# Kernel tuning notes

Measured on AMD Instinct MI355X. Metric: run time of the kernel, lower is better.

Reference implementation:

```python
import jax, jax.numpy as jnp
import numpy as np

N = 128
INSTANCES = 64
EMBED_DIM = 256
HIDDEN = 1024
BATCH = 2048


def _kaiming(key, dims):
    # matches custom_kaiming: randn * sqrt(2 / dims[-2])
    return jax.random.normal(key, dims, dtype=jnp.float32) * np.sqrt(2.0 / float(dims[-2])).astype(np.float32)


def setup_inputs() -> dict:
    key = jax.random.key(0)
    k_a, k_el, k_er, k_lin, k_un = jax.random.split(key, 5)
    a = jax.random.randint(k_a, (BATCH, 2), 0, N, dtype=jnp.int64 if jax.config.jax_enable_x64 else jnp.int32)
    return {
        "a": a,
        "embedding_left": _kaiming(k_el, (INSTANCES, N, EMBED_DIM)),
        "embedding_right": _kaiming(k_er, (INSTANCES, N, EMBED_DIM)),
        "linear": _kaiming(k_lin, (INSTANCES, EMBED_DIM, HIDDEN)),
        "unembedding": _kaiming(k_un, (INSTANCES, HIDDEN, N)),
    }


def reference(a, embedding_left, embedding_right, linear, unembedding):
    # one-hot @ embedding == direct gather along the vocab axis (same math, O(1) per lookup)
    a1, a2 = a[:, 0], a[:, 1]
    # [instances, batch, embed] -> [batch, instances, embed]
    x1 = jnp.transpose(jnp.take(embedding_left, a1, axis=1), (1, 0, 2))
    x2 = jnp.transpose(jnp.take(embedding_right, a2, axis=1), (1, 0, 2))
    hidden = jnp.einsum('bie,ieh->bih', x1 + x2, linear)
    out = jnp.einsum('bih,ihn->bin', jax.nn.gelu(hidden, approximate=False), unembedding)
    return out
```

## Files before the change

### kernel.cpp

```cpp
#include <hip/hip_runtime.h>
#include <hip/hip_bf16.h>

typedef __bf16 bf16;
typedef __bf16 bf16x8 __attribute__((ext_vector_type(8)));
typedef float  f32x4  __attribute__((ext_vector_type(4)));

#define MFMA16(A,B,C) __builtin_amdgcn_mfma_f32_16x16x32_bf16((A),(B),(C),0,0,0)

constexpr int NI    = 64;
constexpr int NN    = 128;
constexpr int E     = 256;
constexpr int HID   = 1024;
constexpr int BATCH = 2048;
constexpr int BM    = 128;
constexpr int BH    = 64;
constexpr int W1P   = E  + 8;
constexpr int W2P   = BH + 8;
constexpr int HP    = BH + 8;

__global__ __launch_bounds__(256) void transpose_cvt(
    const float* __restrict__ in, bf16* __restrict__ out, int R, int C)
{
    __shared__ bf16 t[64][74];
    const int inst = blockIdx.z;
    const int r0 = blockIdx.y * 64, c0 = blockIdx.x * 64;
    const float* ip = in + ((size_t)inst * R + r0) * C + c0;
    #pragma unroll
    for (int it = 0; it < 4; ++it) {
        int idx = it * 256 + threadIdx.x;
        int r = idx >> 4, c4 = idx & 15;
        f32x4 v = *(const f32x4*)(ip + (size_t)r * C + c4 * 4);
        #pragma unroll
        for (int k = 0; k < 4; ++k) t[r][c4 * 4 + k] = (bf16)v[k];
    }
    __syncthreads();
    bf16* op = out + ((size_t)inst * C + c0) * R + r0;
    #pragma unroll
    for (int it = 0; it < 2; ++it) {
        int idx = it * 256 + threadIdx.x;
        int c = idx >> 3, r8 = idx & 7;
        bf16x8 tmp;
        #pragma unroll
        for (int k = 0; k < 8; ++k) tmp[k] = t[r8 * 8 + k][c];
        *(bf16x8*)(op + (size_t)c * R + r8 * 8) = tmp;
    }
}

__device__ __forceinline__ float fast_gelu(float x) {
    float p = 1.5957691216f * __builtin_fmaf(0.044715f * x * x, x, x);
    return x * __builtin_amdgcn_rcpf(1.0f + __expf(-p));
}

template <bool PRET>
__global__ __launch_bounds__(256, 2) void mlp3_fused(
    const int*   __restrict__ a,
    const float* __restrict__ embL,
    const float* __restrict__ embR,
    const void*  __restrict__ W1v,
    const void*  __restrict__ W2v,
    float* __restrict__ out)
{
    __shared__ __align__(16) bf16 sW1[BH][W1P];
    __shared__ __align__(16) bf16 sW2[NN][W2P];
    __shared__ __align__(16) bf16 sH [BM][HP];
    static_assert(sizeof(bf16) * (BH * W1P + NN * W2P + BM * HP) <= 80 * 1024, "2 blocks/CU");

    const int blk   = blockIdx.x;
    const int xcd   = blk & 7;
    const int j     = blk >> 3;
    const int inst  = xcd + 8 * (j >> 4);
    const int btile = j & 15;

    const int tid  = threadIdx.x;
    const int wave = tid >> 6;
    const int lane = tid & 63;
    const int m = lane & 15;
    const int q = lane >> 4;

    bf16x8 aF[2][8];
    #pragma unroll
    for (int rt = 0; rt < 2; ++rt) {
        const int r  = btile * BM + wave * 32 + rt * 16 + m;
        const int i1 = a[2 * r + 0];
        const int i2 = a[2 * r + 1];
        const float* pl = embL + ((size_t)inst * NN + i1) * E;
        const float* pr = embR + ((size_t)inst * NN + i2) * E;
        #pragma unroll
        for (int ks = 0; ks < 8; ++ks) {
            const int e0 = ks * 32 + q * 8;
            f32x4 l0 = *(const f32x4*)(pl + e0);
            f32x4 l1 = *(const f32x4*)(pl + e0 + 4);
            f32x4 r0 = *(const f32x4*)(pr + e0);
            f32x4 r1 = *(const f32x4*)(pr + e0 + 4);
            bf16x8 s;
            #pragma unroll
            for (int k = 0; k < 4; ++k) {
                s[k]     = (bf16)(l0[k] + r0[k]);
                s[k + 4] = (bf16)(l1[k] + r1[k]);
            }
            aF[rt][ks] = s;
        }
    }

    f32x4 O[2][8];
    #pragma unroll
    for (int rt = 0; rt < 2; ++rt)
        #pragma unroll
        for (int ct = 0; ct < 8; ++ct)
            O[rt][ct] = (f32x4){0.f, 0.f, 0.f, 0.f};

    #pragma unroll 1
    for (int c = 0; c < HID / BH; ++c) {
        __syncthreads();
        if (PRET) {
            const bf16* W1 = (const bf16*)W1v;
            const bf16* W2 = (const bf16*)W2v;
            #pragma unroll
            for (int it = 0; it < 8; ++it) {
                const int idx = it * 256 + tid;
                const int hl = idx >> 5, e16 = idx & 31;
                *(bf16x8*)&sW1[hl][e16 * 8] =
                    *(const bf16x8*)(W1 + ((size_t)inst * HID + c * BH + hl) * E + e16 * 8);
            }
            #pragma unroll
            for (int it = 0; it < 4; ++it) {
                const int idx = it * 256 + tid;
                const int n = idx >> 3, h8 = idx & 7;
                *(bf16x8*)&sW2[n][h8 * 8] =
                    *(const bf16x8*)(W2 + ((size_t)inst * NN + n) * HID + c * BH + h8 * 8);
            }
        } else {
            const float* W1 = (const float*)W1v;
            const float* W2 = (const float*)W2v;
            #pragma unroll
            for (int it = 0; it < 8; ++it) {
                const int idx = it * 256 + tid;
                const int e = idx >> 3, h8 = idx & 7;
                f32x4 v0 = *(const f32x4*)(W1 + ((size_t)inst * E + e) * HID + c * BH + h8 * 8);
                f32x4 v1 = *(const f32x4*)(W1 + ((size_t)inst * E + e) * HID + c * BH + h8 * 8 + 4);
                #pragma unroll
                for (int k = 0; k < 4; ++k) {
                    sW1[h8 * 8 + k][e]     = (bf16)v0[k];
                    sW1[h8 * 8 + k + 4][e] = (bf16)v1[k];
                }
            }
            #pragma unroll
            for (int it = 0; it < 4; ++it) {
                const int idx = it * 256 + tid;
                const int h = idx >> 4, n8 = idx & 15;
                f32x4 v0 = *(const f32x4*)(W2 + ((size_t)inst * HID + c * BH + h) * NN + n8 * 8);
                f32x4 v1 = *(const f32x4*)(W2 + ((size_t)inst * HID + c * BH + h) * NN + n8 * 8 + 4);
                #pragma unroll
                for (int k = 0; k < 4; ++k) {
                    sW2[n8 * 8 + k][h]     = (bf16)v0[k];
                    sW2[n8 * 8 + k + 4][h] = (bf16)v1[k];
                }
            }
        }
        __syncthreads();

        f32x4 S[2][4];
        #pragma unroll
        for (int rt = 0; rt < 2; ++rt)
            #pragma unroll
            for (int ct = 0; ct < 4; ++ct) S[rt][ct] = (f32x4){0.f, 0.f, 0.f, 0.f};
        #pragma unroll
        for (int ks = 0; ks < 8; ++ks) {
            #pragma unroll
            for (int ct = 0; ct < 4; ++ct) {
                bf16x8 b = *(const bf16x8*)&sW1[ct * 16 + m][ks * 32 + q * 8];
                S[0][ct] = MFMA16(aF[0][ks], b, S[0][ct]);
                S[1][ct] = MFMA16(aF[1][ks], b, S[1][ct]);
            }
        }

        #pragma unroll
        for (int rt = 0; rt < 2; ++rt)
            #pragma unroll
            for (int ct = 0; ct < 4; ++ct)
                #pragma unroll
                for (int rr = 0; rr < 4; ++rr)
                    sH[wave * 32 + rt * 16 + q * 4 + rr][ct * 16 + m] =
                        (bf16)fast_gelu(S[rt][ct][rr]);
        asm volatile("s_waitcnt lgkmcnt(0)" ::: "memory");

        #pragma unroll
        for (int k2 = 0; k2 < 2; ++k2) {
            bf16x8 h0 = *(const bf16x8*)&sH[wave * 32 +  0 + m][k2 * 32 + q * 8];
            bf16x8 h1 = *(const bf16x8*)&sH[wave * 32 + 16 + m][k2 * 32 + q * 8];
            #pragma unroll
            for (int ct = 0; ct < 8; ++ct) {
                bf16x8 b = *(const bf16x8*)&sW2[ct * 16 + m][k2 * 32 + q * 8];
                O[0][ct] = MFMA16(h0, b, O[0][ct]);
                O[1][ct] = MFMA16(h1, b, O[1][ct]);
            }
        }
    }

    #pragma unroll
    for (int rt = 0; rt < 2; ++rt)
        #pragma unroll
        for (int ct = 0; ct < 8; ++ct)
            #pragma unroll
            for (int rr = 0; rr < 4; ++rr) {
                const int b = btile * BM + wave * 32 + rt * 16 + q * 4 + rr;
                const int n = ct * 16 + m;
                out[((size_t)b * NI + inst) * NN + n] = O[rt][ct][rr];
            }
}

extern "C" void kernel_launch(void* const* d_in, const int* in_sizes, int n_in,
                              void* d_out, int out_size, void* d_ws, size_t ws_size,
                              hipStream_t stream)
{
    const int*   a    = (const int*)d_in[0];
    const float* embL = (const float*)d_in[1];
    const float* embR = (const float*)d_in[2];
    const float* lin  = (const float*)d_in[3];
    const float* une  = (const float*)d_in[4];
    float* out = (float*)d_out;

    const size_t w1t_elems = (size_t)NI * HID * E;
    const size_t w2t_elems = (size_t)NI * NN * HID;
    const size_t need = (w1t_elems + w2t_elems) * sizeof(bf16);

    const int nblocks = (BATCH / BM) * NI;

    if (ws_size >= need) {
        bf16* w1t = (bf16*)d_ws;
        bf16* w2t = w1t + w1t_elems;
        transpose_cvt<<<dim3(HID / 64, E / 64, NI), 256, 0, stream>>>(
            lin, w1t, E, HID);
        transpose_cvt<<<dim3(NN / 64, HID / 64, NI), 256, 0, stream>>>(
            une, w2t, HID, NN);
        mlp3_fused<true><<<nblocks, 256, 0, stream>>>(
            a, embL, embR, (const void*)w1t, (const void*)w2t, out);
    } else {
        mlp3_fused<false><<<nblocks, 256, 0, stream>>>(
            a, embL, embR, (const void*)lin, (const void*)une, out);
    }
}
```

Measured before the change: 315.2 us.

## Pre-swizzle weights for direct global-to-LDS loads and keep GELU hidden in registers

The transpose kernels are replaced with pack kernels that write W1 and W2 in XOR-swizzled bf16 layouts. These match the MFMA fragment order, so the fused kernel can copy tiles straight into LDS with global_load_lds and skip the register round trip. The first GEMM now computes the transpose (weights as A operand). Its output is passed through GELU and fed directly as the A fragment of the second GEMM, which removes the sH shared-memory staging buffer. The smaller LDS footprint allows three blocks per CU, at the cost of higher register pressure and more complex packing kernels.

```diff
diff --git a/kernel.cpp b/kernel.cpp
--- a/kernel.cpp
+++ b/kernel.cpp
@@ -3,6 +3,7 @@
 
 typedef __bf16 bf16;
 typedef __bf16 bf16x8 __attribute__((ext_vector_type(8)));
+typedef __bf16 bf16x4 __attribute__((ext_vector_type(4)));
 typedef float  f32x4  __attribute__((ext_vector_type(4)));
 
 #define MFMA16(A,B,C) __builtin_amdgcn_mfma_f32_16x16x32_bf16((A),(B),(C),0,0,0)
@@ -18,32 +19,10 @@
 constexpr int W2P   = BH + 8;
 constexpr int HP    = BH + 8;
 
-__global__ __launch_bounds__(256) void transpose_cvt(
-    const float* __restrict__ in, bf16* __restrict__ out, int R, int C)
-{
-    __shared__ bf16 t[64][74];
-    const int inst = blockIdx.z;
-    const int r0 = blockIdx.y * 64, c0 = blockIdx.x * 64;
-    const float* ip = in + ((size_t)inst * R + r0) * C + c0;
-    #pragma unroll
-    for (int it = 0; it < 4; ++it) {
-        int idx = it * 256 + threadIdx.x;
-        int r = idx >> 4, c4 = idx & 15;
-        f32x4 v = *(const f32x4*)(ip + (size_t)r * C + c4 * 4);
-        #pragma unroll
-        for (int k = 0; k < 4; ++k) t[r][c4 * 4 + k] = (bf16)v[k];
-    }
-    __syncthreads();
-    bf16* op = out + ((size_t)inst * C + c0) * R + r0;
-    #pragma unroll
-    for (int it = 0; it < 2; ++it) {
-        int idx = it * 256 + threadIdx.x;
-        int c = idx >> 3, r8 = idx & 7;
-        bf16x8 tmp;
-        #pragma unroll
-        for (int k = 0; k < 8; ++k) tmp[k] = t[r8 * 8 + k][c];
-        *(bf16x8*)(op + (size_t)c * R + r8 * 8) = tmp;
-    }
+__device__ __forceinline__ void glds16(const void* g, void* l) {
+    __builtin_amdgcn_global_load_lds(
+        (const __attribute__((address_space(1))) unsigned int*)g,
+        (__attribute__((address_space(3))) unsigned int*)l, 16, 0, 0);
 }
 
 __device__ __forceinline__ float fast_gelu(float x) {
@@ -51,19 +30,84 @@
     return x * __builtin_amdgcn_rcpf(1.0f + __expf(-p));
 }
 
-template <bool PRET>
-__global__ __launch_bounds__(256, 2) void mlp3_fused(
+__global__ __launch_bounds__(256) void pack_w1(
+    const float* __restrict__ in, bf16* __restrict__ out)
+{
+    __shared__ __align__(16) bf16 t[64][264];
+    const int inst = blockIdx.y;
+    const int h0   = blockIdx.x * 64;
+    const int tid  = threadIdx.x;
+    {
+        const int hq = tid & 15;
+        const int e0 = tid >> 4;
+        const float* ip = in + (size_t)inst * E * HID + h0 + hq * 4;
+        #pragma unroll
+        for (int it = 0; it < 16; ++it) {
+            int e = it * 16 + e0;
+            f32x4 v = *(const f32x4*)(ip + (size_t)e * HID);
+            #pragma unroll
+            for (int k = 0; k < 4; ++k) t[hq * 4 + k][e] = (bf16)v[k];
+        }
+    }
+    __syncthreads();
+    bf16* op = out + ((size_t)inst * HID + h0) * E;
+    #pragma unroll
+    for (int it = 0; it < 8; ++it) {
+        int o  = it * 256 + tid;
+        int hl = o >> 5, p = o & 31;
+        int tt = p ^ (hl & 7);
+        bf16x8 v = *(const bf16x8*)&t[hl][tt * 8];
+        *(bf16x8*)(op + (size_t)o * 8) = v;
+    }
+}
+
+__global__ __launch_bounds__(256) void pack_w2(
+    const float* __restrict__ in, bf16* __restrict__ out)
+{
+    __shared__ __align__(16) bf16 t[128][68];
+    const int inst = blockIdx.y;
+    const int c    = blockIdx.x;
+    const int tid  = threadIdx.x;
+    {
+        const int nq = tid & 31;
+        const int h0 = tid >> 5;
+        const float* ip = in + ((size_t)inst * HID + c * 64) * NN + nq * 4;
+        #pragma unroll
+        for (int it = 0; it < 8; ++it) {
+            int h = it * 8 + h0;
+            f32x4 v = *(const f32x4*)(ip + (size_t)h * NN);
+            #pragma unroll
+            for (int k = 0; k < 4; ++k) t[nq * 4 + k][h] = (bf16)v[k];
+        }
+    }
+    __syncthreads();
+    bf16* ob = out + (size_t)inst * NN * HID + (size_t)c * 64;
+    #pragma unroll
+    for (int it = 0; it < 4; ++it) {
+        int o = it * 256 + tid;
+        int n = o >> 3, p = o & 7;
+        int tt = p ^ (n & 7);
+        int k2 = tt >> 2, qq = tt & 3;
+        const bf16* r0 = &t[n][k2 * 32 + qq * 4];
+        bf16x4 lo = *(const bf16x4*)r0;
+        bf16x4 hi = *(const bf16x4*)(r0 + 16);
+        bf16x8 v;
+        v[0] = lo[0]; v[1] = lo[1]; v[2] = lo[2]; v[3] = lo[3];
+        v[4] = hi[0]; v[5] = hi[1]; v[6] = hi[2]; v[7] = hi[3];
+        *(bf16x8*)(ob + (size_t)n * 1024 + p * 8) = v;
+    }
+}
+
+__global__ __launch_bounds__(256, 3) void mlp3_fused_v2(
     const int*   __restrict__ a,
     const float* __restrict__ embL,
     const float* __restrict__ embR,
-    const void*  __restrict__ W1v,
-    const void*  __restrict__ W2v,
+    const bf16*  __restrict__ W1,
+    const bf16*  __restrict__ W2,
     float* __restrict__ out)
 {
-    __shared__ __align__(16) bf16 sW1[BH][W1P];
-    __shared__ __align__(16) bf16 sW2[NN][W2P];
-    __shared__ __align__(16) bf16 sH [BM][HP];
-    static_assert(sizeof(bf16) * (BH * W1P + NN * W2P + BM * HP) <= 80 * 1024, "2 blocks/CU");
+    __shared__ __align__(16) bf16 sW1[BH * E];
+    __shared__ __align__(16) bf16 sW2[NN * BH];
 
     const int blk   = blockIdx.x;
     const int xcd   = blk & 7;
@@ -74,8 +118,9 @@
     const int tid  = threadIdx.x;
     const int wave = tid >> 6;
     const int lane = tid & 63;
-    const int m = lane & 15;
-    const int q = lane >> 4;
+    const int m  = lane & 15;
+    const int q  = lane >> 4;
+    const int xm = m & 7;
 
     bf16x8 aF[2][8];
     #pragma unroll
@@ -109,52 +154,155 @@
         for (int ct = 0; ct < 8; ++ct)
             O[rt][ct] = (f32x4){0.f, 0.f, 0.f, 0.f};
 
+    const char* w1g = (const char*)W1 + (size_t)inst * (HID * E * 2);
+    const char* w2g = (const char*)W2 + (size_t)inst * (NN * HID * 2);
+    char* s1 = (char*)sW1;
+    char* s2 = (char*)sW2;
+
     #pragma unroll 1
     for (int c = 0; c < HID / BH; ++c) {
         __syncthreads();
-        if (PRET) {
-            const bf16* W1 = (const bf16*)W1v;
-            const bf16* W2 = (const bf16*)W2v;
+        {
+            const char* g1 = w1g + c * (BH * E * 2);
             #pragma unroll
             for (int it = 0; it < 8; ++it) {
-                const int idx = it * 256 + tid;
-                const int hl = idx >> 5, e16 = idx & 31;
-                *(bf16x8*)&sW1[hl][e16 * 8] =
-                    *(const bf16x8*)(W1 + ((size_t)inst * HID + c * BH + hl) * E + e16 * 8);
-            }
+                const int b = it * 4 + wave;
+                glds16(g1 + b * 1024 + lane * 16, s1 + b * 1024);
+            }
+            const char* g2 = w2g + c * 128;
             #pragma unroll
             for (int it = 0; it < 4; ++it) {
-                const int idx = it * 256 + tid;
-                const int n = idx >> 3, h8 = idx & 7;
-                *(bf16x8*)&sW2[n][h8 * 8] =
-                    *(const bf16x8*)(W2 + ((size_t)inst * NN + n) * HID + c * BH + h8 * 8);
-            }
-        } else {
-            const float* W1 = (const float*)W1v;
-            const float* W2 = (const float*)W2v;
-            #pragma unroll
-            for (int it = 0; it < 8; ++it) {
-                const int idx = it * 256 + tid;
-                const int e = idx >> 3, h8 = idx & 7;
-                f32x4 v0 = *(const f32x4*)(W1 + ((size_t)inst * E + e) * HID + c * BH + h8 * 8);
-                f32x4 v1 = *(const f32x4*)(W1 + ((size_t)inst * E + e) * HID + c * BH + h8 * 8 + 4);
+                const int b = it * 4 + wave;
+                const int n = b * 8 + (lane >> 3);
+                glds16(g2 + (size_t)n * 2048 + (lane & 7) * 16, s2 + b * 1024);
+            }
+        }
+        __syncthreads();
+
+        #pragma unroll
+        for (int k2 = 0; k2 < 2; ++k2) {
+            bf16x8 pa[2];
+            #pragma unroll
+            for (int cth = 0; cth < 2; ++cth) {
+                const int ct = k2 * 2 + cth;
+                f32x4 S0 = (f32x4){0.f, 0.f, 0.f, 0.f};
+                f32x4 S1 = (f32x4){0.f, 0.f, 0.f, 0.f};
                 #pragma unroll
-                for (int k = 0; k < 4; ++k) {
-                    sW1[h8 * 8 + k][e]     = (bf16)v0[k];
-                    sW1[h8 * 8 + k + 4][e] = (bf16)v1[k];
+                for (int ks = 0; ks < 8; ++ks) {
+                    const int sw = ((ks * 4 + q) ^ xm) * 16;
+                    bf16x8 w1f = *(const bf16x8*)(s1 + (ct * 16 + m) * 512 + sw);
+                    S0 = MFMA16(w1f, aF[0][ks], S0);
+                    S1 = MFMA16(w1f, aF[1][ks], S1);
                 }
-            }
-            #pragma unroll
-            for (int it = 0; it < 4; ++it) {
-                const int idx = it * 256 + tid;
-                const int h = idx >> 4, n8 = idx & 15;
-                f32x4 v0 = *(const f32x4*)(W2 + ((size_t)inst * HID + c * BH + h) * NN + n8 * 8);
-                f32x4 v1 = *(const f32x4*)(W2 + ((size_t)inst * HID + c * BH + h) * NN + n8 * 8 + 4);
                 #pragma unroll
-                for (int k = 0; k < 4; ++k) {
-                    sW2[n8 * 8 + k][h]     = (bf16)v0[k];
-                    sW2[n8 * 8 + k + 4][h] = (bf16)v1[k];
+                for (int rr = 0; rr < 4; ++rr) {
+                    pa[0][cth * 4 + rr] = (bf16)fast_gelu(S0[rr]);
+                    pa[1][cth * 4 + rr] = (bf16)fast_gelu(S1[rr]);
                 }
+            }
+            #pragma unroll
+            for (int ct2 = 0; ct2 < 8; ++ct2) {
+                const int sw = ((k2 * 4 + q) ^ xm) * 16;
+                bf16x8 w2f = *(const bf16x8*)(s2 + (ct2 * 16 + m) * 128 + sw);
+                O[0][ct2] = MFMA16(pa[0], w2f, O[0][ct2]);
+                O[1][ct2] = MFMA16(pa[1], w2f, O[1][ct2]);
+            }
+        }
+    }
+
+    #pragma unroll
+    for (int rt = 0; rt < 2; ++rt)
+        #pragma unroll
+        for (int ct = 0; ct < 8; ++ct)
+            #pragma unroll
+            for (int rr = 0; rr < 4; ++rr) {
+                const int b = btile * BM + wave * 32 + rt * 16 + q * 4 + rr;
+                const int n = ct * 16 + m;
+                out[((size_t)b * NI + inst) * NN + n] = O[rt][ct][rr];
+            }
+}
+
+__global__ __launch_bounds__(256, 2) void mlp3_fallback(
+    const int*   __restrict__ a,
+    const float* __restrict__ embL,
+    const float* __restrict__ embR,
+    const float* __restrict__ W1,
+    const float* __restrict__ W2,
+    float* __restrict__ out)
+{
+    __shared__ __align__(16) bf16 sW1[BH][W1P];
+    __shared__ __align__(16) bf16 sW2[NN][W2P];
+    __shared__ __align__(16) bf16 sH [BM][HP];
+
+    const int blk   = blockIdx.x;
+    const int xcd   = blk & 7;
+    const int j     = blk >> 3;
+    const int inst  = xcd + 8 * (j >> 4);
+    const int btile = j & 15;
+
+    const int tid  = threadIdx.x;
+    const int wave = tid >> 6;
+    const int lane = tid & 63;
+    const int m = lane & 15;
+    const int q = lane >> 4;
+
+    bf16x8 aF[2][8];
+    #pragma unroll
+    for (int rt = 0; rt < 2; ++rt) {
+        const int r  = btile * BM + wave * 32 + rt * 16 + m;
+        const int i1 = a[2 * r + 0];
+        const int i2 = a[2 * r + 1];
+        const float* pl = embL + ((size_t)inst * NN + i1) * E;
+        const float* pr = embR + ((size_t)inst * NN + i2) * E;
+        #pragma unroll
+        for (int ks = 0; ks < 8; ++ks) {
+            const int e0 = ks * 32 + q * 8;
+            f32x4 l0 = *(const f32x4*)(pl + e0);
+            f32x4 l1 = *(const f32x4*)(pl + e0 + 4);
+            f32x4 r0 = *(const f32x4*)(pr + e0);
+            f32x4 r1 = *(const f32x4*)(pr + e0 + 4);
+            bf16x8 s;
+            #pragma unroll
+            for (int k = 0; k < 4; ++k) {
+                s[k]     = (bf16)(l0[k] + r0[k]);
+                s[k + 4] = (bf16)(l1[k] + r1[k]);
+            }
+            aF[rt][ks] = s;
+        }
+    }
+
+    f32x4 O[2][8];
+    #pragma unroll
+    for (int rt = 0; rt < 2; ++rt)
+        #pragma unroll
+        for (int ct = 0; ct < 8; ++ct)
+            O[rt][ct] = (f32x4){0.f, 0.f, 0.f, 0.f};
+
+    #pragma unroll 1
+    for (int c = 0; c < HID / BH; ++c) {
+        __syncthreads();
+        #pragma unroll
+        for (int it = 0; it < 8; ++it) {
+            const int idx = it * 256 + tid;
+            const int e = idx >> 3, h8 = idx & 7;
+            f32x4 v0 = *(const f32x4*)(W1 + ((size_t)inst * E + e) * HID + c * BH + h8 * 8);
+            f32x4 v1 = *(const f32x4*)(W1 + ((size_t)inst * E + e) * HID + c * BH + h8 * 8 + 4);
+            #pragma unroll
+            for (int k = 0; k < 4; ++k) {
+                sW1[h8 * 8 + k][e]     = (bf16)v0[k];
+                sW1[h8 * 8 + k + 4][e] = (bf16)v1[k];
+            }
+        }
+        #pragma unroll
+        for (int it = 0; it < 4; ++it) {
+            const int idx = it * 256 + tid;
+            const int h = idx >> 4, n8 = idx & 15;
+            f32x4 v0 = *(const f32x4*)(W2 + ((size_t)inst * HID + c * BH + h) * NN + n8 * 8);
+            f32x4 v1 = *(const f32x4*)(W2 + ((size_t)inst * HID + c * BH + h) * NN + n8 * 8 + 4);
+            #pragma unroll
+            for (int k = 0; k < 4; ++k) {
+                sW2[n8 * 8 + k][h]     = (bf16)v0[k];
+                sW2[n8 * 8 + k + 4][h] = (bf16)v1[k];
             }
         }
         __syncthreads();
@@ -229,14 +377,12 @@
     if (ws_size >= need) {
         bf16* w1t = (bf16*)d_ws;
         bf16* w2t = w1t + w1t_elems;
-        transpose_cvt<<<dim3(HID / 64, E / 64, NI), 256, 0, stream>>>(
-            lin, w1t, E, HID);
-        transpose_cvt<<<dim3(NN / 64, HID / 64, NI), 256, 0, stream>>>(
-            une, w2t, HID, NN);
-        mlp3_fused<true><<<nblocks, 256, 0, stream>>>(
-            a, embL, embR, (const void*)w1t, (const void*)w2t, out);
+        pack_w1<<<dim3(HID / 64, NI), 256, 0, stream>>>(lin, w1t);
+        pack_w2<<<dim3(HID / BH, NI), 256, 0, stream>>>(une, w2t);
+        mlp3_fused_v2<<<nblocks, 256, 0, stream>>>(
+            a, embL, embR, w1t, w2t, out);
     } else {
-        mlp3_fused<false><<<nblocks, 256, 0, stream>>>(
-            a, embL, embR, (const void*)lin, (const void*)une, out);
-    }
-}
+        mlp3_fallback<<<nblocks, 256, 0, stream>>>(
+            a, embL, embR, lin, une, out);
+    }
+}
```

Measured after the change: 325.6 us. 1.03x slower.
